# Optimization experiments

Hardware: AMD Instinct MI355X
Metric: run time of the kernel (lower is better)

## Reference

```python
import jax, jax.numpy as jnp
import numpy as np

B, S, H = 2, 2048, 1024
NH, HD = 16, 64
WIN = 256
EPS = 1e-5


def _layernorm(x, g, b):
    # normalize over last dim (head_dim)
    m = jnp.mean(x, axis=-1, keepdims=True)
    v = jnp.mean((x - m) ** 2, axis=-1, keepdims=True)
    return (x - m) * jax.lax.rsqrt(v + EPS) * g + b


def setup_inputs() -> dict:
    key = jax.random.key(0)
    ks = jax.random.split(key, 6)
    scale = 1.0 / np.sqrt(2.0 * H)  # ~ xavier_uniform with gain 1/sqrt(2)
    inp = {
        "x": jax.random.normal(ks[0], (B, S, H), dtype=jnp.float32),
        "Wq": jax.random.normal(ks[1], (H, H), dtype=jnp.float32) * scale,
        "bq": jnp.zeros((H,), jnp.float32),
        "Wk": jax.random.normal(ks[2], (H, H), dtype=jnp.float32) * scale,
        "bk": jnp.zeros((H,), jnp.float32),
        "Wv": jax.random.normal(ks[3], (H, H), dtype=jnp.float32) * scale,
        "bv": jnp.zeros((H,), jnp.float32),
        "Wo": jax.random.normal(ks[4], (H, H), dtype=jnp.float32) * scale,
        "bo": jnp.zeros((H,), jnp.float32),
        "ln_q_w": jnp.ones((HD,), jnp.float32),
        "ln_q_b": jnp.zeros((HD,), jnp.float32),
        "ln_k_w": jnp.ones((HD,), jnp.float32),
        "ln_k_b": jnp.zeros((HD,), jnp.float32),
    }
    return inp


def reference(x, Wq, bq, Wk, bk, Wv, bv, Wo, bo, ln_q_w, ln_q_b, ln_k_w, ln_k_b):
    b, s, _ = x.shape
    # projections (torch Linear: x @ W.T + b)
    q = (x @ Wq.T + bq).reshape(b, s, NH, HD)
    k = (x @ Wk.T + bk).reshape(b, s, NH, HD)
    v = (x @ Wv.T + bv).reshape(b, s, NH, HD)
    # QK layernorm over head_dim
    q = _layernorm(q, ln_q_w, ln_q_b)
    k = _layernorm(k, ln_k_w, ln_k_b)
    # scores [b, h, s, s]
    scores = jnp.einsum("bqhd,bkhd->bhqk", q, k) / np.sqrt(HD).astype(np.float32)
    i = jnp.arange(s)[:, None]
    j = jnp.arange(s)[None, :]
    mask = (j <= i) & (i - j <= WIN)
    scores = jnp.where(mask[None, None], scores, -jnp.inf)
    probs = jax.nn.softmax(scores, axis=-1)
    out = jnp.einsum("bhqk,bkhd->bqhd", probs, v).reshape(b, s, NH * HD)
    return out @ Wo.T + bo
```

## Files before the change

kernel.cpp:

```cpp
#include <hip/hip_runtime.h>
#include <hip/hip_bf16.h>
#include <cstdint>

typedef __hip_bfloat16 bf16;
typedef __attribute__((ext_vector_type(8))) short s16x8;
typedef __attribute__((ext_vector_type(4))) float f32x4;

#define NB_B 2
#define NB_S 2048
#define NB_H 1024
#define NB_NH 16
#define NB_HD 64
#define NB_WIN 256
#define NTOK 4096

static __device__ __forceinline__ unsigned pack_bf16(float a, float b) {
    bf16 ta = __float2bfloat16(a), tb = __float2bfloat16(b);
    return (unsigned)*(unsigned short*)&ta | ((unsigned)*(unsigned short*)&tb << 16);
}
static __device__ __forceinline__ unsigned short bf16u(float a) {
    bf16 t = __float2bfloat16(a);
    return *(unsigned short*)&t;
}

__global__ void k_castall(const float* __restrict__ x, const float* __restrict__ Wq,
                          const float* __restrict__ Wk, const float* __restrict__ Wv,
                          const float* __restrict__ Wo,
                          bf16* __restrict__ xb, bf16* __restrict__ wqkvb,
                          bf16* __restrict__ wob) {
    int idx = blockIdx.x * blockDim.x + threadIdx.x;
    const float* in; bf16* out; int i;
    if (idx < 1048576)        { in = x;  out = xb;              i = idx * 4; }
    else if (idx < 1310720)   { in = Wq; out = wqkvb;           i = (idx - 1048576) * 4; }
    else if (idx < 1572864)   { in = Wk; out = wqkvb + 1048576; i = (idx - 1310720) * 4; }
    else if (idx < 1835008)   { in = Wv; out = wqkvb + 2097152; i = (idx - 1572864) * 4; }
    else                      { in = Wo; out = wob;             i = (idx - 1835008) * 4; }
    const float4 v = *(const float4*)(in + i);
    ushort4 u;
    u.x = bf16u(v.x); u.y = bf16u(v.y); u.z = bf16u(v.z); u.w = bf16u(v.w);
    *(ushort4*)((unsigned short*)out + i) = u;
}

#define G_STAGE(AD, BD, KT)                                                          \
    do {                                                                             \
        _Pragma("unroll")                                                            \
        for (int it_ = 0; it_ < 4; ++it_) {                                          \
            int c_ = it_ * 256 + tid;                                                \
            int row_ = c_ >> 3, pc_ = c_ & 7;                                        \
            int col_ = ((pc_ ^ (row_ & 7)) << 3);                                    \
            __builtin_amdgcn_global_load_lds(                                        \
                (const __attribute__((address_space(1))) void*)(Ap + (size_t)(m0 + row_) * 1024 + (KT) + col_), \
                (__attribute__((address_space(3))) void*)((AD) + c_ * 8), 16, 0, 0); \
            __builtin_amdgcn_global_load_lds(                                        \
                (const __attribute__((address_space(1))) void*)(Bp + (size_t)(n0 + row_) * 1024 + (KT) + col_), \
                (__attribute__((address_space(3))) void*)((BD) + c_ * 8), 16, 0, 0); \
        }                                                                            \
        __builtin_amdgcn_sched_barrier(0);                                           \
    } while (0)

#define G_COMPUTE(AS, BS)                                                            \
    do {                                                                             \
        _Pragma("unroll")                                                            \
        for (int kk_ = 0; kk_ < 2; ++kk_) {                                          \
            const int rchunk_ = (((kk_ << 2) + g) ^ (q & 7)) << 3;                   \
            s16x8 af_[4], bf_[4];                                                    \
            _Pragma("unroll")                                                        \
            for (int mi_ = 0; mi_ < 4; ++mi_)                                        \
                af_[mi_] = *(const s16x8*)&(AS)[(wr * 64 + mi_ * 16 + q) * 64 + rchunk_]; \
            _Pragma("unroll")                                                        \
            for (int ni_ = 0; ni_ < 4; ++ni_)                                        \
                bf_[ni_] = *(const s16x8*)&(BS)[(wc * 64 + ni_ * 16 + q) * 64 + rchunk_]; \
            __builtin_amdgcn_s_setprio(1);                                           \
            _Pragma("unroll")                                                        \
            for (int mi_ = 0; mi_ < 4; ++mi_)                                        \
                _Pragma("unroll")                                                    \
                for (int ni_ = 0; ni_ < 4; ++ni_)                                    \
                    acc[mi_][ni_] = __builtin_amdgcn_mfma_f32_16x16x32_bf16(         \
                        af_[mi_], bf_[ni_], acc[mi_][ni_], 0, 0, 0);                 \
            __builtin_amdgcn_s_setprio(0);                                           \
        }                                                                            \
    } while (0)

__global__ __launch_bounds__(256) void k_gemm_qkv(const bf16* __restrict__ Ap,
                                                  const bf16* __restrict__ Bp,
                                                  const float* __restrict__ bq,
                                                  const float* __restrict__ bk,
                                                  const float* __restrict__ bv,
                                                  const float* __restrict__ lqw,
                                                  const float* __restrict__ lqb,
                                                  const float* __restrict__ lkw,
                                                  const float* __restrict__ lkb,
                                                  bf16* __restrict__ qbuf,
                                                  bf16* __restrict__ kbuf,
                                                  bf16* __restrict__ vtb) {
    __shared__ bf16 As0[128 * 64], As1[128 * 64];
    __shared__ bf16 Bs0[128 * 64], Bs1[128 * 64];
    const int tid = threadIdx.x;
    const int lane = tid & 63;
    const int w = tid >> 6;
    const int wr = w >> 1, wc = w & 1;

    const int orig = blockIdx.y * gridDim.x + blockIdx.x;
    const int wk = (orig & 7) * 96 + (orig >> 3);
    const int m0 = (wk / 24) * 128, n0 = (wk % 24) * 128;

    const int g = lane >> 4, q = lane & 15;

    f32x4 acc[4][4] = {};

    G_STAGE(As0, Bs0, 0);
    __syncthreads();
#pragma unroll 2
    for (int kt = 0; kt < 1024; kt += 128) {
        G_STAGE(As1, Bs1, kt + 64);
        G_COMPUTE(As0, Bs0);
        __syncthreads();
        if (kt + 128 < 1024) G_STAGE(As0, Bs0, kt + 128);
        G_COMPUTE(As1, Bs1);
        __syncthreads();
    }

    const int col0 = n0 + wc * 64;
    const int hh = col0 >> 6;
    const int csub = col0 & 1023;
    const float* bias = (hh < 16) ? bq : (hh < 32) ? bk : bv;

    float bcol[4];
#pragma unroll
    for (int ni = 0; ni < 4; ++ni) bcol[ni] = bias[csub + ni * 16 + q];
#pragma unroll
    for (int mi = 0; mi < 4; ++mi)
#pragma unroll
        for (int ni = 0; ni < 4; ++ni)
#pragma unroll
            for (int r = 0; r < 4; ++r) acc[mi][ni][r] += bcol[ni];

    if (hh < 32) {
        const float* gwa = (hh < 16) ? lqw : lkw;
        const float* gba = (hh < 16) ? lqb : lkb;
        float gam[4], bet[4];
#pragma unroll
        for (int ni = 0; ni < 4; ++ni) {
            gam[ni] = gwa[ni * 16 + q];
            bet[ni] = gba[ni * 16 + q];
        }
        bf16* outp = (hh < 16) ? qbuf : kbuf;
#pragma unroll
        for (int mi = 0; mi < 4; ++mi)
#pragma unroll
            for (int r = 0; r < 4; ++r) {
                float s1 = acc[mi][0][r] + acc[mi][1][r] + acc[mi][2][r] + acc[mi][3][r];
                float s2 = acc[mi][0][r] * acc[mi][0][r] + acc[mi][1][r] * acc[mi][1][r]
                         + acc[mi][2][r] * acc[mi][2][r] + acc[mi][3][r] * acc[mi][3][r];
#pragma unroll
                for (int mm = 1; mm < 16; mm <<= 1) {
                    s1 += __shfl_xor(s1, mm, 64);
                    s2 += __shfl_xor(s2, mm, 64);
                }
                float mean = s1 * (1.f / 64.f);
                float var = s2 * (1.f / 64.f) - mean * mean;
                float rs = rsqrtf(var + 1e-5f);
                int token = m0 + wr * 64 + mi * 16 + g * 4 + r;
#pragma unroll
                for (int ni = 0; ni < 4; ++ni) {
                    float y = (acc[mi][ni][r] - mean) * rs * gam[ni] + bet[ni];
                    outp[(size_t)token * 1024 + csub + ni * 16 + q] = __float2bfloat16(y);
                }
            }
    } else {
        const int b = m0 >> 11;
        const int bh = b * 16 + (csub >> 6);
        const int sbase0 = (m0 & 2047) + wr * 64 + g * 4;
#pragma unroll
        for (int mi = 0; mi < 4; ++mi) {
            const int sb = sbase0 + mi * 16;
#pragma unroll
            for (int ni = 0; ni < 4; ++ni) {
                const int d = ni * 16 + q;
                ushort4 u;
                u.x = bf16u(acc[mi][ni][0]); u.y = bf16u(acc[mi][ni][1]);
                u.z = bf16u(acc[mi][ni][2]); u.w = bf16u(acc[mi][ni][3]);
                *(ushort4*)(vtb + ((size_t)bh * 64 + d) * 2048 + sb) = u;
            }
        }
    }
}

__global__ __launch_bounds__(256) void k_gemm_out(const bf16* __restrict__ Ap,
                                                  const bf16* __restrict__ Bp,
                                                  const float* __restrict__ bias,
                                                  float* __restrict__ Cv) {
    __shared__ bf16 As0[128 * 64], As1[128 * 64];
    __shared__ bf16 Bs0[128 * 64], Bs1[128 * 64];
    const int tid = threadIdx.x;
    const int lane = tid & 63;
    const int w = tid >> 6;
    const int wr = w >> 1, wc = w & 1;

    const int orig = blockIdx.y * gridDim.x + blockIdx.x;
    const int wk = (orig & 7) * 32 + (orig >> 3);
    const int m0 = (wk / 8) * 128, n0 = (wk % 8) * 128;

    const int g = lane >> 4, q = lane & 15;

    f32x4 acc[4][4] = {};

    G_STAGE(As0, Bs0, 0);
    __syncthreads();
#pragma unroll 2
    for (int kt = 0; kt < 1024; kt += 128) {
        G_STAGE(As1, Bs1, kt + 64);
        G_COMPUTE(As0, Bs0);
        __syncthreads();
        if (kt + 128 < 1024) G_STAGE(As0, Bs0, kt + 128);
        G_COMPUTE(As1, Bs1);
        __syncthreads();
    }

#pragma unroll
    for (int mi = 0; mi < 4; ++mi)
#pragma unroll
        for (int ni = 0; ni < 4; ++ni) {
            int colg = n0 + wc * 64 + ni * 16 + q;
            float bcol = bias[colg];
#pragma unroll
            for (int r = 0; r < 4; ++r) {
                int rowg = m0 + wr * 64 + mi * 16 + g * 4 + r;
                Cv[(size_t)rowg * 1024 + colg] = acc[mi][ni][r] + bcol;
            }
        }
}

#undef G_STAGE
#undef G_COMPUTE

__global__ __launch_bounds__(256) void k_attn(const bf16* __restrict__ qb,
                                              const bf16* __restrict__ kb,
                                              const bf16* __restrict__ vt,
                                              bf16* __restrict__ att) {
    __shared__ bf16 Ks[2][32 * 64];
    __shared__ bf16 Vs[2][64 * 32];

    const int orig = blockIdx.y * gridDim.x + blockIdx.x;
    const int wk = (orig & 7) * 128 + (orig >> 3);
    const int q0 = (wk & 31) * 64;
    const int bh = wk >> 5;

    const int b = bh >> 4, h = bh & 15;
    const int tid = threadIdx.x;
    const int w = tid >> 6;
    const int lane = tid & 63;
    const int g = lane >> 4, qi = lane & 15;
    const int qw0 = q0 + w * 16;
    const int iq = qw0 + qi;

    const size_t qbase = ((size_t)(b * 2048 + iq)) * 1024 + h * 64 + g * 8;
    s16x8 bq0 = *(const s16x8*)(qb + qbase);
    s16x8 bq1 = *(const s16x8*)(qb + qbase + 32);

    f32x4 o[4] = {};
    float lp = 0.f;

    int jmin = q0 - NB_WIN; if (jmin < 0) jmin = 0;
    const int c0 = jmin >> 5;
    const int c1 = (q0 + 63) >> 5;

    const int krow = tid >> 3, kpc = tid & 7;
    const int kcol = ((kpc ^ (krow & 7)) << 3);
    const int vrow = tid >> 2, vpc = tid & 3;
    const int vcol = ((vpc ^ (vrow & 3)) << 3);
    const bf16* kbase = kb + ((size_t)(b * 2048 + krow)) * 1024 + h * 64 + kcol;
    const bf16* vbase = vt + ((size_t)bh * 64 + vrow) * 2048 + vcol;

    __builtin_amdgcn_global_load_lds(
        (const __attribute__((address_space(1))) void*)(kbase + (size_t)(c0 * 32) * 1024),
        (__attribute__((address_space(3))) void*)(&Ks[0][tid * 8]), 16, 0, 0);
    __builtin_amdgcn_global_load_lds(
        (const __attribute__((address_space(1))) void*)(vbase + c0 * 32),
        (__attribute__((address_space(3))) void*)(&Vs[0][tid * 8]), 16, 0, 0);
    __syncthreads();

    int buf = 0;
    for (int c = c0; c <= c1; ++c) {
        const int ks = c * 32;
        if (c < c1) {
            const int ksn = ks + 32;
            __builtin_amdgcn_global_load_lds(
                (const __attribute__((address_space(1))) void*)(kbase + (size_t)ksn * 1024),
                (__attribute__((address_space(3))) void*)(&Ks[buf ^ 1][tid * 8]), 16, 0, 0);
            __builtin_amdgcn_global_load_lds(
                (const __attribute__((address_space(1))) void*)(vbase + ksn),
                (__attribute__((address_space(3))) void*)(&Vs[buf ^ 1][tid * 8]), 16, 0, 0);
        }

        if (ks + 31 >= qw0 - NB_WIN && ks <= qw0 + 15) {
            const int ch0 = ((g ^ (qi & 7)) << 3);
            const bf16* kr0 = &Ks[buf][qi * 64];
            const bf16* kr1 = &Ks[buf][(16 + qi) * 64];
            s16x8 a00 = *(const s16x8*)(kr0 + ch0);
            s16x8 a01 = *(const s16x8*)(kr0 + (ch0 ^ 32));
            s16x8 a10 = *(const s16x8*)(kr1 + ch0);
            s16x8 a11 = *(const s16x8*)(kr1 + (ch0 ^ 32));

            f32x4 s0 = {}, s1 = {};
            s0 = __builtin_amdgcn_mfma_f32_16x16x32_bf16(a00, bq0, s0, 0, 0, 0);
            s0 = __builtin_amdgcn_mfma_f32_16x16x32_bf16(a01, bq1, s0, 0, 0, 0);
            s1 = __builtin_amdgcn_mfma_f32_16x16x32_bf16(a10, bq0, s1, 0, 0, 0);
            s1 = __builtin_amdgcn_mfma_f32_16x16x32_bf16(a11, bq1, s1, 0, 0, 0);

            float p0[4], p1[4];
#pragma unroll
            for (int r = 0; r < 4; ++r) {
                int j0 = ks + 4 * g + r, j1 = j0 + 16;
                p0[r] = ((unsigned)(iq - j0) <= (unsigned)NB_WIN)
                            ? __expf(s0[r] * 0.125f - 8.f) : 0.f;
                p1[r] = ((unsigned)(iq - j1) <= (unsigned)NB_WIN)
                            ? __expf(s1[r] * 0.125f - 8.f) : 0.f;
                lp += p0[r] + p1[r];
            }
            unsigned P0 = pack_bf16(p0[0], p0[1]), P1 = pack_bf16(p0[2], p0[3]);
            unsigned Q0 = pack_bf16(p1[0], p1[1]), Q1 = pack_bf16(p1[2], p1[3]);

            const int srcA = qi + (g & 1) * 32;
            const int srcB = srcA + 16;
            unsigned tP0a = __shfl((int)P0, srcA, 64), tQ0a = __shfl((int)Q0, srcA, 64);
            unsigned tP1a = __shfl((int)P1, srcA, 64), tQ1a = __shfl((int)Q1, srcA, 64);
            unsigned tP0b = __shfl((int)P0, srcB, 64), tQ0b = __shfl((int)Q0, srcB, 64);
            unsigned tP1b = __shfl((int)P1, srcB, 64), tQ1b = __shfl((int)Q1, srcB, 64);
            union { s16x8 v; unsigned u[4]; } pa;
            pa.u[0] = (g < 2) ? tP0a : tQ0a;
            pa.u[1] = (g < 2) ? tP1a : tQ1a;
            pa.u[2] = (g < 2) ? tP0b : tQ0b;
            pa.u[3] = (g < 2) ? tP1b : tQ1b;

            const int chv = ((g ^ (qi & 3)) << 3);
#pragma unroll
            for (int db = 0; db < 4; ++db) {
                s16x8 bv = *(const s16x8*)&Vs[buf][(db * 16 + qi) * 32 + chv];
                o[db] = __builtin_amdgcn_mfma_f32_16x16x32_bf16(pa.v, bv, o[db], 0, 0, 0);
            }
        }

        __syncthreads();
        buf ^= 1;
    }

    float l2 = lp + __shfl_xor(lp, 16, 64);
    float lf = l2 + __shfl_xor(l2, 32, 64);
    float lr[4];
#pragma unroll
    for (int r = 0; r < 4; ++r) lr[r] = __shfl(lf, 4 * g + r, 64);

#pragma unroll
    for (int db = 0; db < 4; ++db)
#pragma unroll
        for (int r = 0; r < 4; ++r) {
            float vlu = o[db][r] / lr[r];
            att[((size_t)(b * 2048 + qw0 + 4 * g + r)) * 1024 + h * 64 + db * 16 + qi] =
                __float2bfloat16(vlu);
        }
}

extern "C" void kernel_launch(void* const* d_in, const int* in_sizes, int n_in,
                              void* d_out, int out_size, void* d_ws, size_t ws_size,
                              hipStream_t stream) {
    const float* x   = (const float*)d_in[0];
    const float* Wq  = (const float*)d_in[1];
    const float* bq  = (const float*)d_in[2];
    const float* Wk  = (const float*)d_in[3];
    const float* bk  = (const float*)d_in[4];
    const float* Wv  = (const float*)d_in[5];
    const float* bv  = (const float*)d_in[6];
    const float* Wo  = (const float*)d_in[7];
    const float* bo  = (const float*)d_in[8];
    const float* lqw = (const float*)d_in[9];
    const float* lqb = (const float*)d_in[10];
    const float* lkw = (const float*)d_in[11];
    const float* lkb = (const float*)d_in[12];

    char* ws = (char*)d_ws;
    bf16* xb    = (bf16*)(ws + 0);
    bf16* wqkvb = (bf16*)(ws + 8388608);
    bf16* wob   = (bf16*)(ws + 14680064);
    bf16* qbuf  = (bf16*)(ws + 16777216);
    bf16* kbuf  = (bf16*)(ws + 25165824);
    bf16* vtb   = (bf16*)(ws + 33554432);
    bf16* attb  = (bf16*)(ws + 41943040);

    k_castall<<<8192, 256, 0, stream>>>(x, Wq, Wk, Wv, Wo, xb, wqkvb, wob);

    k_gemm_qkv<<<dim3(24, 32), 256, 0, stream>>>(xb, wqkvb, bq, bk, bv,
                                                 lqw, lqb, lkw, lkb,
                                                 qbuf, kbuf, vtb);

    k_attn<<<dim3(32, 32), 256, 0, stream>>>(qbuf, kbuf, vtb, attb);

    k_gemm_out<<<dim3(8, 32), 256, 0, stream>>>(attb, wob, bo, (float*)d_out);
}
```

Before: 91.35 us.

## Use explicit vmcnt waits and raw barriers to deepen GEMM and attention prefetch

The GEMM main loop is restructured to keep two LDS stages of global loads in flight, using s_waitcnt vmcnt(8) plus raw s_barrier in place of __syncthreads, which drains all outstanding memory ops. The attention loop likewise waits only for the current chunk's loads (vmcnt(2)) so the next chunk's K/V prefetch stays outstanding across the barrier. The aim is to overlap global-to-LDS traffic with MFMA work. It depends on the exact count of outstanding vector memory ops per stage being right; a wrong vmcnt would silently read stale LDS data.

```diff
diff --git a/kernel.cpp b/kernel.cpp
--- a/kernel.cpp
+++ b/kernel.cpp
@@ -22,6 +22,9 @@
     bf16 t = __float2bfloat16(a);
     return *(unsigned short*)&t;
 }
+
+#define VMCNT(n) asm volatile("s_waitcnt vmcnt(" #n ")" ::: "memory")
+#define SBAR __builtin_amdgcn_s_barrier()
 
 __global__ void k_castall(const float* __restrict__ x, const float* __restrict__ Wq,
                           const float* __restrict__ Wk, const float* __restrict__ Wv,
@@ -81,6 +84,25 @@
         }                                                                            \
     } while (0)
 
+#define G_MAINLOOP                                                                   \
+    G_STAGE(As0, Bs0, 0);                                                            \
+    G_STAGE(As1, Bs1, 64);                                                           \
+    for (int i_ = 0; i_ < 7; ++i_) {                                                 \
+        const int kt_ = i_ * 128;                                                    \
+        VMCNT(8); SBAR;                                                              \
+        G_COMPUTE(As0, Bs0);                                                         \
+        SBAR;                                                                        \
+        G_STAGE(As0, Bs0, kt_ + 128);                                                \
+        VMCNT(8); SBAR;                                                              \
+        G_COMPUTE(As1, Bs1);                                                         \
+        SBAR;                                                                        \
+        G_STAGE(As1, Bs1, kt_ + 192);                                                \
+    }                                                                                \
+    VMCNT(8); SBAR;                                                                  \
+    G_COMPUTE(As0, Bs0);                                                             \
+    VMCNT(0); SBAR;                                                                  \
+    G_COMPUTE(As1, Bs1)
+
 __global__ __launch_bounds__(256) void k_gemm_qkv(const bf16* __restrict__ Ap,
                                                   const bf16* __restrict__ Bp,
                                                   const float* __restrict__ bq,
@@ -108,17 +130,7 @@
 
     f32x4 acc[4][4] = {};
 
-    G_STAGE(As0, Bs0, 0);
-    __syncthreads();
-#pragma unroll 2
-    for (int kt = 0; kt < 1024; kt += 128) {
-        G_STAGE(As1, Bs1, kt + 64);
-        G_COMPUTE(As0, Bs0);
-        __syncthreads();
-        if (kt + 128 < 1024) G_STAGE(As0, Bs0, kt + 128);
-        G_COMPUTE(As1, Bs1);
-        __syncthreads();
-    }
+    G_MAINLOOP;
 
     const int col0 = n0 + wc * 64;
     const int hh = col0 >> 6;
@@ -205,17 +217,7 @@
 
     f32x4 acc[4][4] = {};
 
-    G_STAGE(As0, Bs0, 0);
-    __syncthreads();
-#pragma unroll 2
-    for (int kt = 0; kt < 1024; kt += 128) {
-        G_STAGE(As1, Bs1, kt + 64);
-        G_COMPUTE(As0, Bs0);
-        __syncthreads();
-        if (kt + 128 < 1024) G_STAGE(As0, Bs0, kt + 128);
-        G_COMPUTE(As1, Bs1);
-        __syncthreads();
-    }
+    G_MAINLOOP;
 
 #pragma unroll
     for (int mi = 0; mi < 4; ++mi)
@@ -233,6 +235,7 @@
 
 #undef G_STAGE
 #undef G_COMPUTE
+#undef G_MAINLOOP
 
 __global__ __launch_bounds__(256) void k_attn(const bf16* __restrict__ qb,
                                               const bf16* __restrict__ kb,
@@ -278,7 +281,6 @@
     __builtin_amdgcn_global_load_lds(
         (const __attribute__((address_space(1))) void*)(vbase + c0 * 32),
         (__attribute__((address_space(3))) void*)(&Vs[0][tid * 8]), 16, 0, 0);
-    __syncthreads();
 
     int buf = 0;
     for (int c = c0; c <= c1; ++c) {
@@ -291,7 +293,12 @@
             __builtin_amdgcn_global_load_lds(
                 (const __attribute__((address_space(1))) void*)(vbase + ksn),
                 (__attribute__((address_space(3))) void*)(&Vs[buf ^ 1][tid * 8]), 16, 0, 0);
-        }
+            __builtin_amdgcn_sched_barrier(0);
+            VMCNT(2);
+        } else {
+            VMCNT(0);
+        }
+        SBAR;
 
         if (ks + 31 >= qw0 - NB_WIN && ks <= qw0 + 15) {
             const int ch0 = ((g ^ (qi & 7)) << 3);
@@ -341,7 +348,7 @@
             }
         }
 
-        __syncthreads();
+        SBAR;
         buf ^= 1;
     }
 
```

Measured after the change: 89.88 us, median of 2. No clear change (-1.6%).
